# Performance work log

Hardware: AMD Instinct MI355X
Metric: run time of the kernel (lower is better)

Reference implementation:

```python
import jax, jax.numpy as jnp
import numpy as np

N_NODES = 100000
N_EDGES = 1600000
NUM_GRAPHS = 1024
IN_FEAT = 7
H = 128
NUM_LAYERS = 3
NUM_CLASSES = 2
BN_EPS = 1e-5


def _lin_init(key, fan_in, fan_out):
    kw, kb = jax.random.split(key)
    s = 1.0 / np.sqrt(fan_in)
    return (jax.random.normal(kw, (fan_in, fan_out), jnp.float32) * s,
            jax.random.normal(kb, (fan_out,), jnp.float32) * s)


def setup_inputs() -> dict:
    key = jax.random.key(0)
    ks = jax.random.split(key, 16)
    x = jax.random.normal(ks[0], (N_NODES, IN_FEAT), jnp.float32)
    edge_index = jax.random.randint(ks[1], (2, N_EDGES), 0, N_NODES, jnp.int32)
    batch = jnp.sort(jax.random.randint(ks[2], (N_NODES,), 0, NUM_GRAPHS, jnp.int32))

    inp = {"x": x, "edge_index": edge_index, "batch": batch}
    # GIN conv MLPs: layer 0 maps IN_FEAT->H->H, layers 1,2 map H->H->H
    fan = [IN_FEAT, H, H]
    for l in range(NUM_LAYERS):
        w1, b1 = _lin_init(ks[3 + 2 * l], fan[l], H)
        w2, b2 = _lin_init(ks[4 + 2 * l], H, H)
        inp[f"w1_{l}"], inp[f"b1_{l}"] = w1, b1
        inp[f"w2_{l}"], inp[f"b2_{l}"] = w2, b2
    # classifier MLP: [3*H, 2*H] + batchnorm(eval) + relu + [2*H, NUM_CLASSES]
    inp["clf_w1"], inp["clf_b1"] = _lin_init(ks[10], NUM_LAYERS * H, 2 * H)
    inp["clf_w2"], inp["clf_b2"] = _lin_init(ks[11], 2 * H, NUM_CLASSES)
    inp["bn_gamma"] = jnp.ones((2 * H,), jnp.float32)
    inp["bn_beta"] = jnp.zeros((2 * H,), jnp.float32)
    inp["bn_mean"] = jax.random.normal(ks[12], (2 * H,), jnp.float32) * 0.1
    inp["bn_var"] = jax.random.uniform(ks[13], (2 * H,), jnp.float32) + 0.5
    return inp


def _gin_conv(h, src, dst, w1, b1, w2, b2):
    # message = gather from source nodes, aggregate = scatter-sum onto target nodes
    agg = jax.ops.segment_sum(h[src], dst, num_segments=N_NODES)
    z = (1.0 + 0.0) * h + agg  # eps = 0 (train_eps=False)
    z = jax.nn.relu(z @ w1 + b1)  # dropout inside MLP is identity in eval
    return z @ w2 + b2


def reference(x, edge_index, batch,
              w1_0, b1_0, w2_0, b2_0,
              w1_1, b1_1, w2_1, b2_1,
              w1_2, b1_2, w2_2, b2_2,
              clf_w1, clf_b1, clf_w2, clf_b2,
              bn_gamma, bn_beta, bn_mean, bn_var):
    src, dst = edge_index[0], edge_index[1]
    params = [(w1_0, b1_0, w2_0, b2_0),
              (w1_1, b1_1, w2_1, b2_1),
              (w1_2, b1_2, w2_2, b2_2)]
    h = x
    xs = []
    for (w1, b1, w2, b2) in params:
        h = _gin_conv(h, src, dst, w1, b1, w2, b2)
        h = jax.nn.relu(h)  # BasicGNN post-conv act (dropout off in eval)
        xs.append(h)
    h = jnp.concatenate(xs, axis=-1)  # jk='cat' -> [N, 3H]
    g = jax.ops.segment_sum(h, batch, num_segments=NUM_GRAPHS)  # global_add_pool
    z = g @ clf_w1 + clf_b1
    z = (z - bn_mean) * jax.lax.rsqrt(bn_var + BN_EPS) * bn_gamma + bn_beta
    z = jax.nn.relu(z)
    return z @ clf_w2 + clf_b2  # [NUM_GRAPHS, NUM_CLASSES]
```

## Files before the change

kernel.cpp:

```cpp
#include <hip/hip_runtime.h>

#define N_NODESC    100000
#define N_EDGESC    1600000
#define NUM_GRAPHSC 1024
#define IN_FEATC    7
#define HDIM        128
#define N_TENSORS   20

#define NB       391
#define CHUNK_A  6250
#define NPADB    391

typedef short s16x8 __attribute__((ext_vector_type(8)));
typedef float f32x4 __attribute__((ext_vector_type(4)));
typedef unsigned short u16x8 __attribute__((ext_vector_type(8)));

#if defined(__has_builtin)
# if __has_builtin(__builtin_amdgcn_cvt_pk_f32_fp8) && __has_builtin(__builtin_amdgcn_cvt_pk_fp8_f32)
#  define USE_HW_FP8 1
# endif
#endif

__global__ void GINModel_15058155340592_kernel() {
}

__device__ __forceinline__ float b2f(unsigned short u){
  union { unsigned int i; float f; } v;
  v.i = ((unsigned int)u) << 16;
  return v.f;
}
__device__ __forceinline__ unsigned short f2b(float f){
  union { float f; unsigned int i; } v;
  v.f = f;
  unsigned int x = v.i;
  return (unsigned short)((x + 0x7fffu + ((x >> 16) & 1u)) >> 16);
}

__device__ __forceinline__ unsigned char enc_fp8(float h){
  float x = fminf(h * 0.125f, 448.f);
#ifdef USE_HW_FP8
  int r = __builtin_amdgcn_cvt_pk_fp8_f32(x, x, 0, false);
  return (unsigned char)(r & 0xFF);
#else
  union { float f; unsigned int i; } u; u.f = x;
  unsigned b = u.i;
  b += 0x7FFFF + ((b >> 20) & 1);
  int e = (int)((b >> 23) & 0xFF) - 120;
  unsigned m = (b >> 20) & 7;
  if (e <= 0) return 0;
  if (e > 15) return 0x7E;
  return (unsigned char)((e << 3) | m);
#endif
}

__device__ __forceinline__ void acc_fp8x4(unsigned int u, float* a){
#ifdef USE_HW_FP8
  auto lo = __builtin_amdgcn_cvt_pk_f32_fp8((int)u, false);
  auto hi = __builtin_amdgcn_cvt_pk_f32_fp8((int)u, true);
  a[0] += lo[0]; a[1] += lo[1]; a[2] += hi[0]; a[3] += hi[1];
#else
  #pragma unroll
  for (int k = 0; k < 4; ++k){
    unsigned b = (u >> (k * 8)) & 0xFF;
    unsigned e = (b >> 3) & 0xF;
    unsigned m = b & 7;
    union { unsigned int i; float f; } w;
    w.i = ((e + 120) << 23) | (m << 20);
    float v = (e == 0) ? (float)m * 0.001953125f : w.f;
    a[k] += v;
  }
#endif
}

__device__ __forceinline__ void acc_bf4(uint2 v, float& a0, float& a1,
                                        float& a2, float& a3){
  union { unsigned int i; float f; } t;
  t.i = v.x << 16;          a0 += t.f;
  t.i = v.x & 0xffff0000u;  a1 += t.f;
  t.i = v.y << 16;          a2 += t.f;
  t.i = v.y & 0xffff0000u;  a3 += t.f;
}

__global__ void k_detect(const unsigned short* xb, int* flag, int* bcnt){
  __shared__ int sh[256];
  int t = threadIdx.x;
  for (int i = t; i < 512; i += 256) bcnt[i] = 0;
  int cnt = 0;
  for (int i = t; i < 512; i += 256){
    unsigned e = (xb[i] >> 7) & 0xFF;
    if (e >= 0x68 && e <= 0x85) ++cnt;
  }
  sh[t] = cnt;
  __syncthreads();
  for (int s = 128; s > 0; s >>= 1){
    if (t < s) sh[t] += sh[t + s];
    __syncthreads();
  }
  if (t == 0) *flag = (sh[0] >= 400) ? 1 : 0;
}

struct CvtDesc { const void* src; int n; int off; };
struct CvtTable { CvtDesc d[N_TENSORS]; int total; };

__global__ void k_bhist(const int* dst, int* bcnt){
  __shared__ int h[NB];
  int tid = threadIdx.x;
  for (int i = tid; i < NB; i += 256) h[i] = 0;
  __syncthreads();
  int beg = blockIdx.x * CHUNK_A;
  int end = beg + CHUNK_A < N_EDGESC ? beg + CHUNK_A : N_EDGESC;
  for (int e = beg + tid; e < end; e += 256)
    atomicAdd(&h[dst[e] >> 8], 1);
  __syncthreads();
  for (int i = tid; i < NB; i += 256)
    if (h[i]) atomicAdd(&bcnt[i], h[i]);
}

__global__ void k_c2(const int* bcnt, int* bbase, int* bcursor, int* rowstart,
                     const int* batch, int* gs){
  if (blockIdx.x == 0){
    __shared__ int sh[512];
    int t = threadIdx.x;
    int v = (t < NB) ? bcnt[t] : 0;
    sh[t] = v;
    __syncthreads();
    for (int off = 1; off < 512; off <<= 1){
      int a = (t >= off) ? sh[t - off] : 0;
      __syncthreads();
      sh[t] += a;
      __syncthreads();
    }
    int excl = sh[t] - v;
    if (t < NB){ bbase[t] = excl; bcursor[t] = excl; }
    if (t == NB) bbase[NB] = sh[t];
    if (t == 0) rowstart[N_NODESC] = N_EDGESC;
  } else {
    int n = (blockIdx.x - 1) * 512 + threadIdx.x;
    if (n >= N_NODESC) return;
    int b = batch[n];
    if (n == 0){
      for (int g = 0; g <= b; ++g) gs[g] = 0;
    } else {
      int pb = batch[n - 1];
      if (pb != b){
        for (int g = pb + 1; g <= b; ++g) gs[g] = n;
      }
    }
    if (n == N_NODESC - 1){
      for (int g = b + 1; g <= NUM_GRAPHSC; ++g) gs[g] = N_NODESC;
    }
  }
}

__global__ void k_bscatter(const int* src, const int* dst, int* bcursor,
                           unsigned int* barr){
  __shared__ int lhist[NB];
  __shared__ int lbase[NB];
  int tid = threadIdx.x;
  for (int i = tid; i < NB; i += 256) lhist[i] = 0;
  __syncthreads();
  int beg = blockIdx.x * CHUNK_A;
  int end = beg + CHUNK_A < N_EDGESC ? beg + CHUNK_A : N_EDGESC;
  for (int e = beg + tid; e < end; e += 256)
    atomicAdd(&lhist[dst[e] >> 8], 1);
  __syncthreads();
  for (int b = tid; b < NB; b += 256){
    int c = lhist[b];
    lbase[b] = c ? atomicAdd(&bcursor[b], c) : 0;
  }
  __syncthreads();
  for (int i = tid; i < NB; i += 256) lhist[i] = 0;
  __syncthreads();
  for (int e = beg + tid; e < end; e += 256){
    int d = dst[e];
    int b = d >> 8;
    int ofs = atomicAdd(&lhist[b], 1);
    barr[lbase[b] + ofs] = ((unsigned)(d & 255) << 17) | (unsigned)src[e];
  }
}

__global__ void k_c4(const unsigned int* barr, const int* bbase,
                     int* rowstart, int* csr,
                     CvtTable T, unsigned short* pool, const int* flag,
                     int ncvtb, const void* xin, unsigned short* x8){
  if (blockIdx.x < NB){
    __shared__ int h[256];
    __shared__ int sc[256];
    __shared__ int cur[256];
    int tid = threadIdx.x;
    int b = blockIdx.x;
    int beg = bbase[b];
    int end = bbase[b + 1];
    int n0 = b << 8;
    h[tid] = 0;
    __syncthreads();
    for (int i = beg + tid; i < end; i += 256)
      atomicAdd(&h[barr[i] >> 17], 1);
    __syncthreads();
    int v = h[tid];
    sc[tid] = v;
    __syncthreads();
    for (int off = 1; off < 256; off <<= 1){
      int a = (tid >= off) ? sc[tid - off] : 0;
      __syncthreads();
      sc[tid] += a;
      __syncthreads();
    }
    int excl = sc[tid] - v;
    int node = n0 + tid;
    if (node < N_NODESC) rowstart[node] = beg + excl;
    cur[tid] = beg + excl;
    __syncthreads();
    for (int i = beg + tid; i < end; i += 256){
      unsigned int e = barr[i];
      int local = e >> 17;
      int slot = atomicAdd(&cur[local], 1);
      csr[slot] = (int)(e & 0x1FFFF) << 7;
    }
  } else {
    int bx = blockIdx.x - NB;
    if (bx < ncvtb){
      int i = bx * 256 + threadIdx.x;
      if (i >= T.total) return;
      int isbf = *flag;
      for (int j = 0; j < N_TENSORS; ++j){
        int o = T.d[j].off;
        if (i >= o && i < o + T.d[j].n){
          int k = i - o;
          if (isbf) pool[i] = ((const unsigned short*)T.d[j].src)[k];
          else      pool[i] = f2b(((const float*)T.d[j].src)[k]);
          return;
        }
      }
    } else {
      int n = (bx - ncvtb) * 256 + threadIdx.x;
      if (n >= N_NODESC) return;
      u16x8 o;
      if (*flag){
        const unsigned short* s = (const unsigned short*)xin + (size_t)n * IN_FEATC;
        #pragma unroll
        for (int j = 0; j < IN_FEATC; ++j) o[j] = s[j];
      } else {
        const float* s = (const float*)xin + (size_t)n * IN_FEATC;
        #pragma unroll
        for (int j = 0; j < IN_FEATC; ++j) o[j] = f2b(s[j]);
      }
      o[7] = 0;
      *(u16x8*)(x8 + (size_t)n * 8) = o;
    }
  }
}

__global__ __launch_bounds__(256)
void k_l0(const unsigned short* x8, const int* rs, const int* csr,
          const unsigned short* w1, const unsigned short* b1,
          unsigned short* t){
  __shared__ __align__(16) float sz[128 * 8];
  int tid  = threadIdx.x;
  int lane = tid & 63;
  int wave = tid >> 6;
  int p    = tid & 1;
  int bn   = tid >> 1;
  int n    = blockIdx.x * 128 + bn;

  int c0 = lane * 2;
  float wa[IN_FEATC], wb[IN_FEATC];
  #pragma unroll
  for (int k = 0; k < IN_FEATC; ++k){
    unsigned int u = *(const unsigned int*)(w1 + k * HDIM + c0);
    union { unsigned int i; float f; } lo, hi;
    lo.i = u << 16; hi.i = u & 0xffff0000u;
    wa[k] = lo.f; wb[k] = hi.f;
  }
  unsigned int ub = *(const unsigned int*)(b1 + c0);
  union { unsigned int i; float f; } blo, bhi;
  blo.i = ub << 16; bhi.i = ub & 0xffff0000u;
  float bv0 = blo.f, bv1 = bhi.f;

  float a0 = 0.f, a1 = 0.f, a2 = 0.f, a3 = 0.f;
  int beg = 0, end = 0;
  if (n < N_NODESC){ beg = rs[n]; end = rs[n + 1]; }
  const unsigned char* xb = (const unsigned char*)x8 + p * 8;
  int i = beg;
  for (; i + 4 <= end; i += 4){
    int o0 = csr[i + 0];
    int o1 = csr[i + 1];
    int o2 = csr[i + 2];
    int o3 = csr[i + 3];
    uint2 v0 = *(const uint2*)(xb + (o0 >> 3));
    uint2 v1 = *(const uint2*)(xb + (o1 >> 3));
    uint2 v2 = *(const uint2*)(xb + (o2 >> 3));
    uint2 v3 = *(const uint2*)(xb + (o3 >> 3));
    acc_bf4(v0, a0, a1, a2, a3);
    acc_bf4(v1, a0, a1, a2, a3);
    acc_bf4(v2, a0, a1, a2, a3);
    acc_bf4(v3, a0, a1, a2, a3);
  }
  for (; i < end; ++i){
    uint2 v = *(const uint2*)(xb + (csr[i] >> 3));
    acc_bf4(v, a0, a1, a2, a3);
  }
  if (n < N_NODESC){
    uint2 v = *(const uint2*)((const unsigned char*)x8 + (size_t)n * 16 + p * 8);
    acc_bf4(v, a0, a1, a2, a3);
  }
  *(f32x4*)&sz[bn * 8 + p * 4] = f32x4{a0, a1, a2, a3};
  __syncthreads();

  int j0 = wave * 32;
  for (int j = 0; j < 32; ++j){
    int no = blockIdx.x * 128 + j0 + j;
    f32x4 z0 = *(const f32x4*)&sz[(j0 + j) * 8];
    f32x4 z1 = *(const f32x4*)&sz[(j0 + j) * 8 + 4];
    float acc0 = bv0, acc1 = bv1;
    acc0 += z0[0] * wa[0]; acc1 += z0[0] * wb[0];
    acc0 += z0[1] * wa[1]; acc1 += z0[1] * wb[1];
    acc0 += z0[2] * wa[2]; acc1 += z0[2] * wb[2];
    acc0 += z0[3] * wa[3]; acc1 += z0[3] * wb[3];
    acc0 += z1[0] * wa[4]; acc1 += z1[0] * wb[4];
    acc0 += z1[1] * wa[5]; acc1 += z1[1] * wb[5];
    acc0 += z1[2] * wa[6]; acc1 += z1[2] * wb[6];
    if (no < N_NODESC){
      unsigned int pk = ((unsigned)f2b(fmaxf(acc1, 0.f)) << 16)
                      | (unsigned)f2b(fmaxf(acc0, 0.f));
      *(unsigned int*)(t + ((size_t)no << 7) + c0) = pk;
    }
  }
}

__global__ __launch_bounds__(256, 2)
void k_gemm128m(const unsigned short* A, const unsigned short* W,
                const unsigned short* bias, unsigned short* C, int ntiles)
{
  int wave = threadIdx.x >> 6;
  int lane = threadIdx.x & 63;
  int quad = lane >> 4;
  int l16  = lane & 15;

  union BU { s16x8 v; unsigned short s[8]; };
  BU bf[4][8];
  #pragma unroll
  for (int ks = 0; ks < 4; ++ks)
    #pragma unroll
    for (int ct = 0; ct < 8; ++ct){
      int c = l16 * 8 + ct;
      #pragma unroll
      for (int j = 0; j < 8; ++j)
        bf[ks][ct].s[j] = W[(ks * 32 + quad * 8 + j) * HDIM + c];
    }

  float bv[8];
  #pragma unroll
  for (int ct = 0; ct < 8; ++ct) bv[ct] = b2f(bias[l16 * 8 + ct]);

  for (int tile = blockIdx.x; tile < ntiles; tile += gridDim.x){
    int r = tile * 64 + wave * 16 + l16;
    BU af[4];
    if (r < N_NODESC){
      const unsigned short* arow = A + (size_t)r * HDIM;
      #pragma unroll
      for (int ks = 0; ks < 4; ++ks)
        af[ks].v = *reinterpret_cast<const s16x8*>(arow + ks * 32 + quad * 8);
    } else {
      #pragma unroll
      for (int ks = 0; ks < 4; ++ks)
        #pragma unroll
        for (int j = 0; j < 8; ++j) af[ks].s[j] = 0;
    }
    f32x4 acc[8];
    #pragma unroll
    for (int ct = 0; ct < 8; ++ct) acc[ct] = f32x4{0.f, 0.f, 0.f, 0.f};
    #pragma unroll
    for (int ks = 0; ks < 4; ++ks)
      #pragma unroll
      for (int ct = 0; ct < 8; ++ct)
        acc[ct] = __builtin_amdgcn_mfma_f32_16x16x32_bf16(af[ks].v, bf[ks][ct].v,
                                                          acc[ct], 0, 0, 0);

    int orow = tile * 64 + wave * 16 + quad * 4;
    #pragma unroll
    for (int rr = 0; rr < 4; ++rr){
      int row = orow + rr;
      if (row < N_NODESC){
        u16x8 o;
        #pragma unroll
        for (int ct = 0; ct < 8; ++ct)
          o[ct] = f2b(fmaxf(acc[ct][rr] + bv[ct], 0.f));
        *(u16x8*)(C + ((size_t)row << 7) + l16 * 8) = o;
      }
    }
  }
}

__global__ void k_agg128(const unsigned short* hin, const unsigned char* t8,
                         const int* rs, const int* csr, unsigned short* zout){
  int lane = threadIdx.x & 63;
  int slot = lane >> 4;
  int fl   = lane & 15;
  int n = blockIdx.x * 16 + (threadIdx.x >> 6) * 4 + slot;
  const unsigned char* hb8 = t8 + fl * 8;
  int beg = rs[n];
  int end = rs[n + 1];
  float a[8] = {0.f, 0.f, 0.f, 0.f, 0.f, 0.f, 0.f, 0.f};
  int i = beg;
  for (; i + 4 <= end; i += 4){
    int o0 = csr[i + 0];
    int o1 = csr[i + 1];
    int o2 = csr[i + 2];
    int o3 = csr[i + 3];
    uint2 v0 = *(const uint2*)(hb8 + o0);
    uint2 v1 = *(const uint2*)(hb8 + o1);
    uint2 v2 = *(const uint2*)(hb8 + o2);
    uint2 v3 = *(const uint2*)(hb8 + o3);
    acc_fp8x4(v0.x, a); acc_fp8x4(v0.y, a + 4);
    acc_fp8x4(v1.x, a); acc_fp8x4(v1.y, a + 4);
    acc_fp8x4(v2.x, a); acc_fp8x4(v2.y, a + 4);
    acc_fp8x4(v3.x, a); acc_fp8x4(v3.y, a + 4);
  }
  for (; i < end; ++i){
    int o = csr[i];
    uint2 v = *(const uint2*)(hb8 + o);
    acc_fp8x4(v.x, a); acc_fp8x4(v.y, a + 4);
  }
  u16x8 vs = *(const u16x8*)(hin + ((size_t)n << 7) + fl * 8);
  u16x8 o;
  #pragma unroll
  for (int j = 0; j < 8; ++j) o[j] = f2b(a[j] * 8.f + b2f(vs[j]));
  *(u16x8*)(zout + ((size_t)n << 7) + fl * 8) = o;
}

__global__ void k_poolA(const unsigned short* __restrict__ h,
                        const int* __restrict__ gs,
                        float* __restrict__ pooled, int coloff,
                        unsigned char* __restrict__ c8){
  __shared__ float red16[16][136];
  int g = blockIdx.x;
  int t = threadIdx.x;
  int r = t >> 4;
  int c = t & 15;
  int s = gs[g];
  int e = gs[g + 1];
  float pa[8] = {0.f, 0.f, 0.f, 0.f, 0.f, 0.f, 0.f, 0.f};
  if (c8){
    for (int n = s + r; n < e; n += 16){
      u16x8 hv = *(const u16x8*)(h + ((size_t)n << 7) + c * 8);
      unsigned int w0 = (unsigned)enc_fp8(b2f(hv[0]))
                      | ((unsigned)enc_fp8(b2f(hv[1])) << 8)
                      | ((unsigned)enc_fp8(b2f(hv[2])) << 16)
                      | ((unsigned)enc_fp8(b2f(hv[3])) << 24);
      unsigned int w1 = (unsigned)enc_fp8(b2f(hv[4]))
                      | ((unsigned)enc_fp8(b2f(hv[5])) << 8)
                      | ((unsigned)enc_fp8(b2f(hv[6])) << 16)
                      | ((unsigned)enc_fp8(b2f(hv[7])) << 24);
      *(uint2*)(c8 + ((size_t)n << 7) + c * 8) = uint2{w0, w1};
      #pragma unroll
      for (int j = 0; j < 8; ++j) pa[j] += b2f(hv[j]);
    }
  } else {
    for (int n = s + r; n < e; n += 16){
      u16x8 hv = *(const u16x8*)(h + ((size_t)n << 7) + c * 8);
      #pragma unroll
      for (int j = 0; j < 8; ++j) pa[j] += b2f(hv[j]);
    }
  }
  #pragma unroll
  for (int j = 0; j < 8; ++j) red16[r][c * 8 + j] = pa[j];
  __syncthreads();
  if (t < 128){
    float ssum = 0.f;
    #pragma unroll
    for (int k = 0; k < 16; ++k) ssum += red16[k][t];
    pooled[(size_t)g * 384 + coloff + t] = ssum;
  }
}

__global__ void k_poolclf(const unsigned short* __restrict__ h,
                          const int* __restrict__ gs,
                          const float* __restrict__ pooled,
                          const unsigned short* w1, const unsigned short* b1,
                          const unsigned short* w2, const unsigned short* b2c,
                          const unsigned short* gamma, const unsigned short* beta,
                          const unsigned short* mean, const unsigned short* var,
                          void* dout, const int* flag){
  __shared__ float red16[16][136];
  __shared__ float sg[384];
  __shared__ float st[256];
  __shared__ float red[256];
  int g = blockIdx.x;
  int t = threadIdx.x;
  int r = t >> 4;
  int c = t & 15;
  int s = gs[g];
  int e = gs[g + 1];
  float pa[8] = {0.f, 0.f, 0.f, 0.f, 0.f, 0.f, 0.f, 0.f};
  for (int n = s + r; n < e; n += 16){
    u16x8 hv = *(const u16x8*)(h + ((size_t)n << 7) + c * 8);
    #pragma unroll
    for (int j = 0; j < 8; ++j) pa[j] += b2f(hv[j]);
  }
  #pragma unroll
  for (int j = 0; j < 8; ++j) red16[r][c * 8 + j] = pa[j];
  sg[t] = pooled[(size_t)g * 384 + t];
  __syncthreads();
  if (t < 128){
    float ssum = 0.f;
    #pragma unroll
    for (int k = 0; k < 16; ++k) ssum += red16[k][t];
    sg[256 + t] = ssum;
  }
  __syncthreads();

  const unsigned short* wp = w1 + t;
  float acc = b2f(b1[t]);
  #pragma unroll 4
  for (int k = 0; k < 384; ++k) acc += sg[k] * b2f(wp[k * 256]);
  float zb = (acc - b2f(mean[t])) * rsqrtf(b2f(var[t]) + 1e-5f) * b2f(gamma[t]) + b2f(beta[t]);
  st[t] = fmaxf(zb, 0.f);
  __syncthreads();
  for (int cc = 0; cc < 2; ++cc){
    red[t] = st[t] * b2f(w2[t * 2 + cc]);
    __syncthreads();
    for (int ss = 128; ss > 0; ss >>= 1){
      if (t < ss) red[t] += red[t + ss];
      __syncthreads();
    }
    if (t == 0){
      float v = red[0] + b2f(b2c[cc]);
      if (*flag) ((unsigned short*)dout)[g * 2 + cc] = f2b(v);
      else       ((float*)dout)[g * 2 + cc] = v;
    }
    __syncthreads();
  }
}

extern "C" void kernel_launch(void* const* d_in, const int* in_sizes, int n_in,
                              void* d_out, int out_size, void* d_ws, size_t ws_size,
                              hipStream_t stream)
{
  const int* ei    = (const int*)d_in[1];
  const int* batch = (const int*)d_in[2];
  (void)n_in; (void)out_size; (void)ws_size;

  char* w = (char*)d_ws;
  int* bcnt     = (int*)(w + 0);
  int* bbase    = (int*)(w + 2048);
  int* bcursor  = (int*)(w + 4096);
  int* rowstart = (int*)(w + 6144);
  int* gstart   = (int*)(w + 406272);
  int* flag     = (int*)(w + 410624);
  unsigned int* barr = (unsigned int*)(w + 410752);
  int* csr      = (int*)(w + 6810752);
  unsigned short* bufP = (unsigned short*)(w + 13210752);
  unsigned short* bufQ = (unsigned short*)(w + 38810752);
  unsigned short* pool = (unsigned short*)(w + 64410752);
  unsigned char* t8    = (unsigned char*)(w + 66410752);
  float* pooled = (float*)(w + 79210752);
  unsigned short* x8 = (unsigned short*)(w + 80783616);

  static const int order[N_TENSORS] =
      {3, 4, 5, 6, 7, 8, 9, 10, 11, 12, 13, 14, 15, 16, 17, 18, 19, 20, 21, 22};
  CvtTable T;
  const unsigned short* pp[23];
  int off = 0;
  for (int j = 0; j < N_TENSORS; ++j){
    int i = order[j];
    T.d[j].src = d_in[i];
    T.d[j].n = in_sizes[i];
    T.d[j].off = off;
    pp[i] = pool + off;
    off += in_sizes[i];
  }
  T.total = off;

  const unsigned short* pw1[3] = {pp[3], pp[7],  pp[11]};
  const unsigned short* pb1[3] = {pp[4], pp[8],  pp[12]};
  const unsigned short* pw2[3] = {pp[5], pp[9],  pp[13]};
  const unsigned short* pb2[3] = {pp[6], pp[10], pp[14]};

  const int* src = ei;
  const int* dst = ei + N_EDGESC;
  int ntiles = (N_NODESC + 63) / 64;
  int ncvt = (T.total + 255) / 256;
  int nc2 = 1 + (N_NODESC + 511) / 512;

  k_detect<<<dim3(1), dim3(256), 0, stream>>>((const unsigned short*)d_in[0], flag, bcnt);

  k_bhist<<<dim3(256), dim3(256), 0, stream>>>(dst, bcnt);
  k_c2<<<dim3(nc2), dim3(512), 0, stream>>>(bcnt, bbase, bcursor, rowstart, batch, gstart);
  k_bscatter<<<dim3(256), dim3(256), 0, stream>>>(src, dst, bcursor, barr);
  k_c4<<<dim3(NB + ncvt + NPADB), dim3(256), 0, stream>>>(barr, bbase, rowstart, csr,
                                                          T, pool, flag, ncvt, d_in[0], x8);

  k_l0<<<dim3((N_NODESC + 127) / 128), dim3(256), 0, stream>>>(x8, rowstart, csr, pw1[0], pb1[0], bufP);
  k_gemm128m<<<dim3(782), dim3(256), 0, stream>>>(bufP, pw2[0], pb2[0], bufP, ntiles);
  k_poolA<<<dim3(NUM_GRAPHSC), dim3(256), 0, stream>>>(bufP, gstart, pooled, 0, t8);

  k_agg128<<<dim3(N_NODESC / 16), dim3(256), 0, stream>>>(bufP, t8, rowstart, csr, bufQ);
  k_gemm128m<<<dim3(782), dim3(256), 0, stream>>>(bufQ, pw1[1], pb1[1], bufQ, ntiles);
  k_gemm128m<<<dim3(782), dim3(256), 0, stream>>>(bufQ, pw2[1], pb2[1], bufQ, ntiles);
  k_poolA<<<dim3(NUM_GRAPHSC), dim3(256), 0, stream>>>(bufQ, gstart, pooled, 128, t8);

  k_agg128<<<dim3(N_NODESC / 16), dim3(256), 0, stream>>>(bufQ, t8, rowstart, csr, bufP);
  k_gemm128m<<<dim3(782), dim3(256), 0, stream>>>(bufP, pw1[2], pb1[2], bufP, ntiles);
  k_gemm128m<<<dim3(782), dim3(256), 0, stream>>>(bufP, pw2[2], pb2[2], bufP, ntiles);
  k_poolclf<<<dim3(NUM_GRAPHSC), dim3(256), 0, stream>>>(bufP, gstart, pooled,
                                                         pp[15], pp[16], pp[17], pp[18],
                                                         pp[19], pp[20], pp[21], pp[22],
                                                         d_out, flag);
}
```

Before: 369.6 us.

## Fuse neighbor aggregation with first MLP GEMM via shared-memory tile

Replaces the separate aggregation kernel and first GEMM of layers 1 and 2 with one kernel. Each block gathers FP8 neighbor features for 64 nodes, writes the bf16 sums into shared memory, then runs MFMA with W1 and applies bias plus ReLU. This removes a global write and re-read of the N×128 intermediate and one launch per layer. The cost is fewer blocks (one per 64-row tile instead of per 16 nodes), a heavy register load from holding all of W1 in registers while gathering, and launch_bounds capping occupancy, which may hurt latency hiding for the irregular gather.

```diff
diff --git a/kernel.cpp b/kernel.cpp
--- a/kernel.cpp
+++ b/kernel.cpp
@@ -392,41 +392,100 @@
   }
 }
 
-__global__ void k_agg128(const unsigned short* hin, const unsigned char* t8,
-                         const int* rs, const int* csr, unsigned short* zout){
+__global__ __launch_bounds__(256, 2)
+void k_aggmm(const unsigned short* hin, const unsigned char* t8,
+             const int* rs, const int* csr,
+             const unsigned short* W, const unsigned short* bias,
+             unsigned short* C)
+{
+  __shared__ __align__(16) unsigned short z[64 * 136];
+  int wave = threadIdx.x >> 6;
   int lane = threadIdx.x & 63;
-  int slot = lane >> 4;
-  int fl   = lane & 15;
-  int n = blockIdx.x * 16 + (threadIdx.x >> 6) * 4 + slot;
-  const unsigned char* hb8 = t8 + fl * 8;
-  int beg = rs[n];
-  int end = rs[n + 1];
-  float a[8] = {0.f, 0.f, 0.f, 0.f, 0.f, 0.f, 0.f, 0.f};
-  int i = beg;
-  for (; i + 4 <= end; i += 4){
-    int o0 = csr[i + 0];
-    int o1 = csr[i + 1];
-    int o2 = csr[i + 2];
-    int o3 = csr[i + 3];
-    uint2 v0 = *(const uint2*)(hb8 + o0);
-    uint2 v1 = *(const uint2*)(hb8 + o1);
-    uint2 v2 = *(const uint2*)(hb8 + o2);
-    uint2 v3 = *(const uint2*)(hb8 + o3);
-    acc_fp8x4(v0.x, a); acc_fp8x4(v0.y, a + 4);
-    acc_fp8x4(v1.x, a); acc_fp8x4(v1.y, a + 4);
-    acc_fp8x4(v2.x, a); acc_fp8x4(v2.y, a + 4);
-    acc_fp8x4(v3.x, a); acc_fp8x4(v3.y, a + 4);
-  }
-  for (; i < end; ++i){
-    int o = csr[i];
-    uint2 v = *(const uint2*)(hb8 + o);
-    acc_fp8x4(v.x, a); acc_fp8x4(v.y, a + 4);
-  }
-  u16x8 vs = *(const u16x8*)(hin + ((size_t)n << 7) + fl * 8);
-  u16x8 o;
-  #pragma unroll
-  for (int j = 0; j < 8; ++j) o[j] = f2b(a[j] * 8.f + b2f(vs[j]));
-  *(u16x8*)(zout + ((size_t)n << 7) + fl * 8) = o;
+  int quad = lane >> 4;
+  int l16  = lane & 15;
+  int tile = blockIdx.x;
+
+  union BU { s16x8 v; unsigned short s[8]; };
+  BU bf[4][8];
+  #pragma unroll
+  for (int ks = 0; ks < 4; ++ks)
+    #pragma unroll
+    for (int ct = 0; ct < 8; ++ct){
+      int c = l16 * 8 + ct;
+      #pragma unroll
+      for (int j = 0; j < 8; ++j)
+        bf[ks][ct].s[j] = W[(ks * 32 + quad * 8 + j) * HDIM + c];
+    }
+  float bv[8];
+  #pragma unroll
+  for (int ct = 0; ct < 8; ++ct) bv[ct] = b2f(bias[l16 * 8 + ct]);
+
+  const unsigned char* hb8 = t8 + l16 * 8;
+  for (int it = 0; it < 4; ++it){
+    int row = wave * 16 + quad * 4 + it;
+    int n = tile * 64 + row;
+    u16x8 o;
+    if (n < N_NODESC){
+      int beg = rs[n];
+      int end = rs[n + 1];
+      float a[8] = {0.f, 0.f, 0.f, 0.f, 0.f, 0.f, 0.f, 0.f};
+      int i = beg;
+      for (; i + 4 <= end; i += 4){
+        int o0 = csr[i + 0];
+        int o1 = csr[i + 1];
+        int o2 = csr[i + 2];
+        int o3 = csr[i + 3];
+        uint2 v0 = *(const uint2*)(hb8 + o0);
+        uint2 v1 = *(const uint2*)(hb8 + o1);
+        uint2 v2 = *(const uint2*)(hb8 + o2);
+        uint2 v3 = *(const uint2*)(hb8 + o3);
+        acc_fp8x4(v0.x, a); acc_fp8x4(v0.y, a + 4);
+        acc_fp8x4(v1.x, a); acc_fp8x4(v1.y, a + 4);
+        acc_fp8x4(v2.x, a); acc_fp8x4(v2.y, a + 4);
+        acc_fp8x4(v3.x, a); acc_fp8x4(v3.y, a + 4);
+      }
+      for (; i < end; ++i){
+        uint2 v = *(const uint2*)(hb8 + csr[i]);
+        acc_fp8x4(v.x, a); acc_fp8x4(v.y, a + 4);
+      }
+      u16x8 vs = *(const u16x8*)(hin + ((size_t)n << 7) + l16 * 8);
+      #pragma unroll
+      for (int j = 0; j < 8; ++j) o[j] = f2b(a[j] * 8.f + b2f(vs[j]));
+    } else {
+      #pragma unroll
+      for (int j = 0; j < 8; ++j) o[j] = 0;
+    }
+    *(u16x8*)&z[row * 136 + l16 * 8] = o;
+  }
+  __syncthreads();
+
+  BU af[4];
+  #pragma unroll
+  for (int ks = 0; ks < 4; ++ks)
+    af[ks].v = *reinterpret_cast<const s16x8*>(
+        &z[(wave * 16 + l16) * 136 + ks * 32 + quad * 8]);
+  f32x4 acc[8];
+  #pragma unroll
+  for (int ct = 0; ct < 8; ++ct) acc[ct] = f32x4{0.f, 0.f, 0.f, 0.f};
+  #pragma unroll
+  for (int ks = 0; ks < 4; ++ks)
+    #pragma unroll
+    for (int ct = 0; ct < 8; ++ct)
+      acc[ct] = __builtin_amdgcn_mfma_f32_16x16x32_bf16(af[ks].v, bf[ks][ct].v,
+                                                        acc[ct], 0, 0, 0);
+
+  int orow = tile * 64 + wave * 16 + quad * 4;
+  #pragma unroll
+  for (int rr = 0; rr < 4; ++rr){
+    int row = orow + rr;
+    if (row < N_NODESC){
+      u16x8 o;
+      #pragma unroll
+      for (int ct = 0; ct < 8; ++ct)
+        o[ct] = f2b(fmaxf(acc[ct][rr] + bv[ct], 0.f));
+      *(u16x8*)(C + ((size_t)row << 7) + l16 * 8) = o;
+    }
+  }
 }
 
 __global__ void k_poolA(const unsigned short* __restrict__ h,
@@ -595,13 +654,13 @@
   k_gemm128m<<<dim3(782), dim3(256), 0, stream>>>(bufP, pw2[0], pb2[0], bufP, ntiles);
   k_poolA<<<dim3(NUM_GRAPHSC), dim3(256), 0, stream>>>(bufP, gstart, pooled, 0, t8);
 
-  k_agg128<<<dim3(N_NODESC / 16), dim3(256), 0, stream>>>(bufP, t8, rowstart, csr, bufQ);
-  k_gemm128m<<<dim3(782), dim3(256), 0, stream>>>(bufQ, pw1[1], pb1[1], bufQ, ntiles);
+  k_aggmm<<<dim3(ntiles), dim3(256), 0, stream>>>(bufP, t8, rowstart, csr,
+                                                  pw1[1], pb1[1], bufQ);
   k_gemm128m<<<dim3(782), dim3(256), 0, stream>>>(bufQ, pw2[1], pb2[1], bufQ, ntiles);
   k_poolA<<<dim3(NUM_GRAPHSC), dim3(256), 0, stream>>>(bufQ, gstart, pooled, 128, t8);
 
-  k_agg128<<<dim3(N_NODESC / 16), dim3(256), 0, stream>>>(bufQ, t8, rowstart, csr, bufP);
-  k_gemm128m<<<dim3(782), dim3(256), 0, stream>>>(bufP, pw1[2], pb1[2], bufP, ntiles);
+  k_aggmm<<<dim3(ntiles), dim3(256), 0, stream>>>(bufQ, t8, rowstart, csr,
+                                                  pw1[2], pb1[2], bufP);
   k_gemm128m<<<dim3(782), dim3(256), 0, stream>>>(bufP, pw2[2], pb2[2], bufP, ntiles);
   k_poolclf<<<dim3(NUM_GRAPHSC), dim3(256), 0, stream>>>(bufP, gstart, pooled,
                                                          pp[15], pp[16], pp[17], pp[18],
```

After: 473.6 us. +28.2%, slower.
